# Performance work log

Measured on AMD Instinct MI355X. Metric: run time of the kernel, lower is better.

## Reference

```python
import jax, jax.numpy as jnp
import numpy as np


def setup_inputs() -> dict:
    key = jax.random.key(0)
    k1, k2, k3, k4 = jax.random.split(key, 4)
    b, s, h, z = 4, 4096, 2048, 64
    scale = 1.0 / np.sqrt(h)
    return {
        "hidden_states": jax.random.normal(k1, (b, s, h), dtype=jnp.float32),
        # nn.Linear(h, z, bias=False): store as (h, z) so y = x @ W
        "Wq": jax.random.normal(k2, (h, z), dtype=jnp.float32) * scale,
        "Wk": jax.random.normal(k3, (h, z), dtype=jnp.float32) * scale,
        "Wv": jax.random.normal(k4, (h, z), dtype=jnp.float32) * scale,
    }


def reference(hidden_states, Wq, Wk, Wv):
    b, s, h = hidden_states.shape
    z = Wq.shape[1]
    # Three small projections: (b, s, z), cast to float32 as in original
    q = jnp.einsum("bsh,hz->bsz", hidden_states, Wq).astype(jnp.float32)
    k = jnp.einsum("bsh,hz->bsz", hidden_states, Wk).astype(jnp.float32)
    v = jnp.einsum("bsh,hz->bsz", hidden_states, Wv).astype(jnp.float32)
    # Per-token outer product over the expert dim: (b, s, z, z)
    attn = q[..., :, None] * k[..., None, :]
    attn = jax.nn.softmax(attn, axis=-1)
    # Weighted sum over the key expert axis j: out[..., i] = sum_j attn[..., i, j] * v[..., j]
    out = jnp.einsum("bsij,bsj->bsi", attn, v)
    return out.reshape(b * s, z)
```

## Files before the change

kernel.cpp:

```cpp
#include <hip/hip_runtime.h>


typedef __bf16 bf16x8 __attribute__((ext_vector_type(8)));
typedef float f32x4  __attribute__((ext_vector_type(4)));

#define NTOK   16384
#define HDIM   2048
#define NCHUNK 64
#define CH_STRIDE (12 * 2 * 512)

__global__ void pack_w_kernel(const float* __restrict__ Wq,
                              const float* __restrict__ Wk,
                              const float* __restrict__ Wv,
                              __bf16* __restrict__ bfrag)
{
  int u = blockIdx.x * blockDim.x + threadIdx.x;
  if (u >= NCHUNK * 12 * 64) return;
  int l  = u & 63;
  int tn = (u >> 6) % 12;
  int c  = u / (12 * 64);
  int n  = tn * 16 + (l & 15);
  int kb = c * 32 + ((l >> 4) << 3);
  const float* W = (n < 64) ? Wq : (n < 128) ? Wk : Wv;
  int nn = n & 63;
  bf16x8 hi, lo;
#pragma unroll
  for (int j = 0; j < 8; ++j) {
    float f = W[(size_t)(kb + j) * 64 + nn];
    __bf16 h = (__bf16)f;
    hi[j] = h;
    lo[j] = (__bf16)(f - (float)h);
  }
  size_t base = (size_t)(c * 12 + tn) * 1024 + (size_t)l * 8;
  *(bf16x8*)(bfrag + base)       = hi;
  *(bf16x8*)(bfrag + base + 512) = lo;
}

__global__ __launch_bounds__(256, 2) void router_kernel(
    const float* __restrict__ x,
    const __bf16* __restrict__ bfrag,
    float* __restrict__ out)
{
  const int tok0 = blockIdx.x * 32;
  const int w    = threadIdx.x >> 6;
  const int lane = threadIdx.x & 63;
  const int mr   = lane & 15;
  const int quad = lane >> 4;

  __shared__ float qkv[32 * 196];

  const float*  a0 = x + (size_t)(tok0 + mr) * HDIM + quad * 8;
  const float*  a1 = a0 + 16 * HDIM;
  const __bf16* bp = bfrag + (size_t)(3 * w) * 1024 + (size_t)lane * 8;

  f32x4 acc[2][3];
#pragma unroll
  for (int i = 0; i < 2; ++i)
#pragma unroll
    for (int t = 0; t < 3; ++t)
      acc[i][t] = (f32x4){0.f, 0.f, 0.f, 0.f};

  float4 pA[4];
  bf16x8 pBh[3], pBl[3];
  pA[0] = *(const float4*)(a0);
  pA[1] = *(const float4*)(a0 + 4);
  pA[2] = *(const float4*)(a1);
  pA[3] = *(const float4*)(a1 + 4);
#pragma unroll
  for (int t = 0; t < 3; ++t) {
    pBh[t] = *(const bf16x8*)(bp + (size_t)t * 1024);
    pBl[t] = *(const bf16x8*)(bp + (size_t)t * 1024 + 512);
  }

  for (int c = 0; c < NCHUNK; ++c) {
    float4 A[4]; bf16x8 Bh[3], Bl[3];
#pragma unroll
    for (int i = 0; i < 4; ++i) A[i] = pA[i];
#pragma unroll
    for (int t = 0; t < 3; ++t) { Bh[t] = pBh[t]; Bl[t] = pBl[t]; }

    if (c + 1 < NCHUNK) {
      const float*  na0 = a0 + (c + 1) * 32;
      const float*  na1 = a1 + (c + 1) * 32;
      const __bf16* nbp = bp + (size_t)(c + 1) * CH_STRIDE;
      pA[0] = *(const float4*)(na0);
      pA[1] = *(const float4*)(na0 + 4);
      pA[2] = *(const float4*)(na1);
      pA[3] = *(const float4*)(na1 + 4);
#pragma unroll
      for (int t = 0; t < 3; ++t) {
        pBh[t] = *(const bf16x8*)(nbp + (size_t)t * 1024);
        pBl[t] = *(const bf16x8*)(nbp + (size_t)t * 1024 + 512);
      }
    }

    bf16x8 ah[2], al[2];
#pragma unroll
    for (int i = 0; i < 2; ++i) {
      float av[8] = {A[2*i].x, A[2*i].y, A[2*i].z, A[2*i].w,
                     A[2*i+1].x, A[2*i+1].y, A[2*i+1].z, A[2*i+1].w};
#pragma unroll
      for (int j = 0; j < 8; ++j) {
        __bf16 h = (__bf16)av[j];
        ah[i][j] = h;
        al[i][j] = (__bf16)(av[j] - (float)h);
      }
    }

#pragma unroll
    for (int i = 0; i < 2; ++i)
#pragma unroll
      for (int t = 0; t < 3; ++t) {
        acc[i][t] = __builtin_amdgcn_mfma_f32_16x16x32_bf16(ah[i], Bh[t], acc[i][t], 0, 0, 0);
        acc[i][t] = __builtin_amdgcn_mfma_f32_16x16x32_bf16(al[i], Bh[t], acc[i][t], 0, 0, 0);
        acc[i][t] = __builtin_amdgcn_mfma_f32_16x16x32_bf16(ah[i], Bl[t], acc[i][t], 0, 0, 0);
      }
  }

#pragma unroll
  for (int i = 0; i < 2; ++i)
#pragma unroll
    for (int t = 0; t < 3; ++t) {
      int col = w * 48 + t * 16 + mr;
      int row = i * 16 + quad * 4;
#pragma unroll
      for (int r = 0; r < 4; ++r)
        qkv[(row + r) * 196 + col] = acc[i][t][r];
    }
  __syncthreads();

  const int tt = threadIdx.x >> 3;
  const int g  = threadIdx.x & 7;
  const float* qrow = qkv + tt * 196;
  float qs[8], lsum[8], osum[8];
#pragma unroll
  for (int ii = 0; ii < 8; ++ii) {
    qs[ii]   = qrow[g * 8 + ii] * 1.44269504f;
    lsum[ii] = 0.f;
    osum[ii] = 0.f;
  }
  for (int j = 0; j < 64; ++j) {
    float kj = qrow[64 + j];
    float vj = qrow[128 + j];
#pragma unroll
    for (int ii = 0; ii < 8; ++ii) {
      float e = __builtin_amdgcn_exp2f(qs[ii] * kj);
      lsum[ii] += e;
      osum[ii] = fmaf(e, vj, osum[ii]);
    }
  }
  float4 r0, r1;
  r0.x = osum[0] / lsum[0]; r0.y = osum[1] / lsum[1];
  r0.z = osum[2] / lsum[2]; r0.w = osum[3] / lsum[3];
  r1.x = osum[4] / lsum[4]; r1.y = osum[5] / lsum[5];
  r1.z = osum[6] / lsum[6]; r1.w = osum[7] / lsum[7];
  float* op = out + (size_t)(tok0 + tt) * 64 + g * 8;
  *(float4*)op       = r0;
  *(float4*)(op + 4) = r1;
}

extern "C" void kernel_launch(void* const* d_in, const int* in_sizes, int n_in,
                              void* d_out, int out_size, void* d_ws, size_t ws_size,
                              hipStream_t stream)
{
  const float* x  = (const float*)d_in[0];
  const float* Wq = (const float*)d_in[1];
  const float* Wk = (const float*)d_in[2];
  const float* Wv = (const float*)d_in[3];
  __bf16* bfrag   = (__bf16*)d_ws;
  float*  out     = (float*)d_out;

  pack_w_kernel<<<(NCHUNK * 12 * 64 + 255) / 256, 256, 0, stream>>>(Wq, Wk, Wv, bfrag);
  router_kernel<<<NTOK / 32, 256, 0, stream>>>(x, bfrag, out);
}
```

Baseline: 258.0 us.

## Split K dimension across two wave groups per block and reduce in LDS

```diff
diff --git a/kernel.cpp b/kernel.cpp
--- a/kernel.cpp
+++ b/kernel.cpp
@@ -7,6 +7,7 @@
 #define NTOK   16384
 #define HDIM   2048
 #define NCHUNK 64
+#define KCH    32
 #define CH_STRIDE (12 * 2 * 512)
 
 __global__ void pack_w_kernel(const float* __restrict__ Wq,
@@ -36,7 +37,7 @@
   *(bf16x8*)(bfrag + base + 512) = lo;
 }
 
-__global__ __launch_bounds__(256, 2) void router_kernel(
+__global__ __launch_bounds__(512, 4) void router_kernel(
     const float* __restrict__ x,
     const __bf16* __restrict__ bfrag,
     float* __restrict__ out)
@@ -44,14 +45,17 @@
   const int tok0 = blockIdx.x * 32;
   const int w    = threadIdx.x >> 6;
   const int lane = threadIdx.x & 63;
+  const int kh   = w >> 2;
+  const int wc   = w & 3;
   const int mr   = lane & 15;
   const int quad = lane >> 4;
 
-  __shared__ float qkv[32 * 196];
+  __shared__ float qkv[2][32 * 196];
 
-  const float*  a0 = x + (size_t)(tok0 + mr) * HDIM + quad * 8;
+  const float*  a0 = x + (size_t)(tok0 + mr) * HDIM + quad * 8 + kh * 1024;
   const float*  a1 = a0 + 16 * HDIM;
-  const __bf16* bp = bfrag + (size_t)(3 * w) * 1024 + (size_t)lane * 8;
+  const __bf16* bp = bfrag + (size_t)(kh * KCH) * CH_STRIDE
+                           + (size_t)(3 * wc) * 1024 + (size_t)lane * 8;
 
   f32x4 acc[2][3];
 #pragma unroll
@@ -72,14 +76,14 @@
     pBl[t] = *(const bf16x8*)(bp + (size_t)t * 1024 + 512);
   }
 
-  for (int c = 0; c < NCHUNK; ++c) {
+  for (int c = 0; c < KCH; ++c) {
     float4 A[4]; bf16x8 Bh[3], Bl[3];
 #pragma unroll
     for (int i = 0; i < 4; ++i) A[i] = pA[i];
 #pragma unroll
     for (int t = 0; t < 3; ++t) { Bh[t] = pBh[t]; Bl[t] = pBl[t]; }
 
-    if (c + 1 < NCHUNK) {
+    if (c + 1 < KCH) {
       const float*  na0 = a0 + (c + 1) * 32;
       const float*  na1 = a1 + (c + 1) * 32;
       const __bf16* nbp = bp + (size_t)(c + 1) * CH_STRIDE;
@@ -121,42 +125,40 @@
   for (int i = 0; i < 2; ++i)
 #pragma unroll
     for (int t = 0; t < 3; ++t) {
-      int col = w * 48 + t * 16 + mr;
+      int col = wc * 48 + t * 16 + mr;
       int row = i * 16 + quad * 4;
 #pragma unroll
       for (int r = 0; r < 4; ++r)
-        qkv[(row + r) * 196 + col] = acc[i][t][r];
+        qkv[kh][(row + r) * 196 + col] = acc[i][t][r];
     }
   __syncthreads();
 
-  const int tt = threadIdx.x >> 3;
-  const int g  = threadIdx.x & 7;
-  const float* qrow = qkv + tt * 196;
-  float qs[8], lsum[8], osum[8];
+  const int tt = threadIdx.x >> 4;
+  const int g  = threadIdx.x & 15;
+  const float* q0 = qkv[0] + tt * 196;
+  const float* q1 = qkv[1] + tt * 196;
+  float qs[4], lsum[4], osum[4];
 #pragma unroll
-  for (int ii = 0; ii < 8; ++ii) {
-    qs[ii]   = qrow[g * 8 + ii] * 1.44269504f;
+  for (int ii = 0; ii < 4; ++ii) {
+    qs[ii]   = (q0[g * 4 + ii] + q1[g * 4 + ii]) * 1.44269504f;
     lsum[ii] = 0.f;
     osum[ii] = 0.f;
   }
   for (int j = 0; j < 64; ++j) {
-    float kj = qrow[64 + j];
-    float vj = qrow[128 + j];
+    float kj = q0[64 + j]  + q1[64 + j];
+    float vj = q0[128 + j] + q1[128 + j];
 #pragma unroll
-    for (int ii = 0; ii < 8; ++ii) {
+    for (int ii = 0; ii < 4; ++ii) {
       float e = __builtin_amdgcn_exp2f(qs[ii] * kj);
       lsum[ii] += e;
       osum[ii] = fmaf(e, vj, osum[ii]);
     }
   }
-  float4 r0, r1;
+  float4 r0;
   r0.x = osum[0] / lsum[0]; r0.y = osum[1] / lsum[1];
   r0.z = osum[2] / lsum[2]; r0.w = osum[3] / lsum[3];
-  r1.x = osum[4] / lsum[4]; r1.y = osum[5] / lsum[5];
-  r1.z = osum[6] / lsum[6]; r1.w = osum[7] / lsum[7];
-  float* op = out + (size_t)(tok0 + tt) * 64 + g * 8;
-  *(float4*)op       = r0;
-  *(float4*)(op + 4) = r1;
+  float* op = out + (size_t)(tok0 + tt) * 64 + g * 4;
+  *(float4*)op = r0;
 }
 
 extern "C" void kernel_launch(void* const* d_in, const int* in_sizes, int n_in,
@@ -171,5 +173,5 @@
   float*  out     = (float*)d_out;
 
   pack_w_kernel<<<(NCHUNK * 12 * 64 + 255) / 256, 256, 0, stream>>>(Wq, Wk, Wv, bfrag);
-  router_kernel<<<NTOK / 32, 256, 0, stream>>>(x, bfrag, out);
+  router_kernel<<<NTOK / 32, 512, 0, stream>>>(x, bfrag, out);
 }
```

After: 267.5 us. +3.7%, slower.
